# Kernel tuning notes

Measured on AMD Instinct MI355X. Metric: run time of the kernel, lower is better.

The kernel has to match this reference:

```python
import jax, jax.numpy as jnp
import numpy as np

LAMBDA_TEMP = 20.0
GAMMA = 20.0
MARGIN = 0.05
EPS = 1e-8

B, K, M, D = 128, 256, 8, 128


def _unit(x, axis=-1):
    return x / jnp.linalg.norm(x, axis=axis, keepdims=True)


def setup_inputs() -> dict:
    key = jax.random.key(0)
    k1, k2, k3 = jax.random.split(key, 3)
    v_proj = _unit(jax.random.normal(k1, (B, K, D), dtype=jnp.float32))
    prototypes = _unit(jax.random.normal(k2, (K, M, D), dtype=jnp.float32))
    concept_labels = jax.random.randint(k3, (B, K), 0, 2, dtype=jnp.int64)
    return {"v_proj": v_proj, "concept_labels": concept_labels, "prototypes": prototypes}


def reference(v_proj, concept_labels, prototypes):
    # all-pairs prototype similarities: query vector (b,k) vs prototypes of concept c
    # sims: (B, K, C, M)
    sims = jnp.einsum('bkd,cmd->bkcm', v_proj, prototypes)
    # Eq.6: soft assignment over the M prototypes of each concept
    q = jax.nn.softmax(GAMMA * sims, axis=-1)
    # Eq.7-8: weighted similarity sim_c(v)  -> (B, K, C)
    sim = jnp.sum(q * sims, axis=-1)
    # positive similarity: concept k queried against its own prototypes, plus margin
    sim_pos = jnp.einsum('bkk->bk', sim) + MARGIN  # (B, K)
    # Eq.9: -log( exp(lam*sim_pos) / (sum_c exp(lam*sim_c) + eps) )
    denom = jnp.sum(jnp.exp(LAMBDA_TEMP * sim), axis=-1) + EPS  # (B, K)
    loss_bk = jnp.log(denom) - LAMBDA_TEMP * sim_pos  # (B, K)
    mask = (concept_labels == 1).astype(loss_bk.dtype)
    num_pos = jnp.sum(mask)
    total = jnp.sum(loss_bk * mask)
    return jnp.where(num_pos > 0, total / num_pos, total)
```

## Files before the change

### kernel.cpp

```cpp
#include <hip/hip_runtime.h>

#define NROWS 32768
#define LT 20.0f
#define CHUNKS 16

typedef _Float16 half8 __attribute__((ext_vector_type(8)));
typedef float    f32x4 __attribute__((ext_vector_type(4)));

__device__ __forceinline__ float swz16(float x) {
    return __int_as_float(__builtin_amdgcn_ds_swizzle(__float_as_int(x), 0x401F));
}

#define GLD16(gp, lp) __builtin_amdgcn_global_load_lds( \
    (const __attribute__((address_space(1))) void*)(gp), \
    (__attribute__((address_space(3))) void*)(lp), 16, 0, 0)

__global__ __launch_bounds__(256)
void mpcl_prep(const float* __restrict__ P, _Float16* __restrict__ Pw)
{
    int id   = blockIdx.x * 256 + threadIdx.x;
    int gcol = id >> 4;
    int dblk = id & 15;
    int ch   = gcol >> 7;
    int col  = gcol & 127;
    int key  = (col & 3) | ((col & 8) >> 1);
    int dbs  = (dblk & 8) | ((dblk ^ key) & 7);
    const float* src = P + (size_t)gcol * 128 + dblk * 8;
    float4 a = *(const float4*)src;
    float4 b = *(const float4*)(src + 4);
    half8 hv;
    hv[0] = (_Float16)a.x; hv[1] = (_Float16)a.y;
    hv[2] = (_Float16)a.z; hv[3] = (_Float16)a.w;
    hv[4] = (_Float16)b.x; hv[5] = (_Float16)b.y;
    hv[6] = (_Float16)b.z; hv[7] = (_Float16)b.w;
    *(half8*)&Pw[((size_t)ch * 2048 + col * 16 + dbs) * 8] = hv;
}

__global__ __launch_bounds__(1024)
void mpcl_main(const float* __restrict__ V,
               const int*   __restrict__ labels,
               const _Float16* __restrict__ Pw,
               int* __restrict__ ws,
               float* __restrict__ out)
{
    __shared__ __align__(16) _Float16 Pst[2][2048 * 8];
    __shared__ float sh_denom[128];
    __shared__ float sh_simpos[128];
    __shared__ float sh_red[32];

    int*   gcnt = ws;
    float* gsum = (float*)(ws + 2);

    const int tid  = threadIdx.x;
    const int lane = tid & 63;
    const int w    = tid >> 6;
    const int rg   = w >> 2;
    const int colq = w & 3;
    const int n    = lane & 15;
    const int q    = lane >> 4;
    const int rowbase = blockIdx.x * 128;

    if (tid < 128) { sh_denom[tid] = 0.0f; sh_simpos[tid] = 0.0f; }

    half8 vh[2][4];
#pragma unroll
    for (int rf = 0; rf < 2; ++rf) {
        const float* vr = V + (size_t)(rowbase + rg * 32 + rf * 16 + n) * 128 + q * 8;
#pragma unroll
        for (int c = 0; c < 4; ++c) {
            float4 x0 = *(const float4*)(vr + c * 32);
            float4 x1 = *(const float4*)(vr + c * 32 + 4);
            vh[rf][c][0] = (_Float16)x0.x; vh[rf][c][1] = (_Float16)x0.y;
            vh[rf][c][2] = (_Float16)x0.z; vh[rf][c][3] = (_Float16)x0.w;
            vh[rf][c][4] = (_Float16)x1.x; vh[rf][c][5] = (_Float16)x1.y;
            vh[rf][c][6] = (_Float16)x1.z; vh[rf][c][7] = (_Float16)x1.w;
        }
    }

    const int col1 = colq * 32 + ((n >> 2) << 3) + (n & 3);
    int off1[4];
#pragma unroll
    for (int c = 0; c < 4; ++c) {
        int dblk = c * 4 + q;
        int dbs  = (dblk & 8) | ((dblk ^ (n & 7)) & 7);
        off1[c]  = (col1 * 16 + dbs) * 8;
    }

    const _Float16* gbase = Pw + (size_t)(w * 128 + lane) * 8;
    _Float16* l0 = &Pst[0][(w * 128) * 8];
    _Float16* l1 = &Pst[1][(w * 128) * 8];

    GLD16(gbase,       l0);
    GLD16(gbase + 512, l0 + 512);

    const int rowk0 = (rowbase + rg * 32 + n) & 255;
    const int rowk1 = (rowbase + rg * 32 + 16 + n) & 255;

    float dn[2] = {0.f, 0.f};

#pragma unroll 1
    for (int ch = 0; ch < CHUNKS; ++ch) {
        __syncthreads();

        if (ch < CHUNKS - 1) {
            const _Float16* g = gbase + (size_t)(ch + 1) * 16384;
            _Float16* lnx = (ch & 1) ? l0 : l1;
            GLD16(g,       lnx);
            GLD16(g + 512, lnx + 512);
        }

        const _Float16* base = (ch & 1) ? &Pst[1][0] : &Pst[0][0];

        f32x4 acc1[2] = {{0.f,0.f,0.f,0.f},{0.f,0.f,0.f,0.f}};
        f32x4 acc2[2] = {{0.f,0.f,0.f,0.f},{0.f,0.f,0.f,0.f}};
#pragma unroll
        for (int c = 0; c < 4; ++c) {
            half8 a1 = *(const half8*)&base[off1[c]];
            half8 a2 = *(const half8*)&base[off1[c] + 512];
            acc1[0] = __builtin_amdgcn_mfma_f32_16x16x32_f16(a1, vh[0][c], acc1[0], 0, 0, 0);
            acc1[1] = __builtin_amdgcn_mfma_f32_16x16x32_f16(a1, vh[1][c], acc1[1], 0, 0, 0);
            acc2[0] = __builtin_amdgcn_mfma_f32_16x16x32_f16(a2, vh[0][c], acc2[0], 0, 0, 0);
            acc2[1] = __builtin_amdgcn_mfma_f32_16x16x32_f16(a2, vh[1][c], acc2[1], 0, 0, 0);
        }

        const int cA = ch * 16 + colq * 4 + q;
#pragma unroll
        for (int rf = 0; rf < 2; ++rf) {
            float x0 = acc1[rf][0], x1 = acc1[rf][1], x2 = acc1[rf][2], x3 = acc1[rf][3];
            float x4 = acc2[rf][0], x5 = acc2[rf][1], x6 = acc2[rf][2], x7 = acc2[rf][3];
            float e0 = __expf(LT * x0), e1 = __expf(LT * x1);
            float e2 = __expf(LT * x2), e3 = __expf(LT * x3);
            float e4 = __expf(LT * x4), e5 = __expf(LT * x5);
            float e6 = __expf(LT * x6), e7 = __expf(LT * x7);
            float es = ((e0 + e1) + (e2 + e3)) + ((e4 + e5) + (e6 + e7));
            float ss = fmaf(e0, x0, fmaf(e1, x1, fmaf(e2, x2, e3 * x3)))
                     + fmaf(e4, x4, fmaf(e5, x5, fmaf(e6, x6, e7 * x7)));
            float simc = __fdividef(ss, es);
            dn[rf] += __expf(LT * simc);
            if (cA == (rf ? rowk1 : rowk0))
                sh_simpos[rg * 32 + rf * 16 + n] = simc;
        }
    }

#pragma unroll
    for (int rf = 0; rf < 2; ++rf) {
        float t = dn[rf];
        t += swz16(t);
        t += __shfl_xor(t, 32);
        if (lane < 16)
            atomicAdd(&sh_denom[rg * 32 + rf * 16 + n], t);
    }
    __syncthreads();

    float s = 0.f, cc = 0.f;
    if (tid < 128) {
        int row = rowbase + tid;
        float lp = logf(sh_denom[tid] + 1e-8f) - LT * (sh_simpos[tid] + 0.05f);
        float mk = (labels[row] == 1) ? 1.0f : 0.0f;
        s = lp * mk;
        cc = mk;
    }
#pragma unroll
    for (int off = 32; off >= 1; off >>= 1) {
        s  += __shfl_down(s, off);
        cc += __shfl_down(cc, off);
    }
    if (lane == 0) { sh_red[w] = s; sh_red[16 + w] = cc; }
    __syncthreads();
    if (tid == 0) {
        s = 0.f; cc = 0.f;
#pragma unroll
        for (int i = 0; i < 16; ++i) { s += sh_red[i]; cc += sh_red[16 + i]; }
        atomicAdd(&gsum[0], s);
        atomicAdd(&gsum[1], cc);
        __threadfence();
        int g = __hip_atomic_fetch_add(gcnt, 1,
                                       __ATOMIC_ACQ_REL, __HIP_MEMORY_SCOPE_AGENT);
        if (g == 255) {
            __threadfence();
            float ts = __hip_atomic_load(&gsum[0], __ATOMIC_RELAXED, __HIP_MEMORY_SCOPE_AGENT);
            float tc = __hip_atomic_load(&gsum[1], __ATOMIC_RELAXED, __HIP_MEMORY_SCOPE_AGENT);
            out[0] = (tc > 0.0f) ? (ts / tc) : ts;
        }
    }
}

extern "C" void kernel_launch(void* const* d_in, const int* in_sizes, int n_in,
                              void* d_out, int out_size, void* d_ws, size_t ws_size,
                              hipStream_t stream)
{
    const float* V      = (const float*)d_in[0];
    const int*   labels = (const int*)d_in[1];
    const float* P      = (const float*)d_in[2];
    float* out = (float*)d_out;
    int*   ws  = (int*)d_ws;
    _Float16* Pw = (_Float16*)((char*)d_ws + 512);

    hipMemsetAsync(ws, 0, 16, stream);
    mpcl_prep<<<128, 256, 0, stream>>>(P, Pw);
    mpcl_main<<<256, 1024, 0, stream>>>(V, labels, Pw, ws, out);
}
```

Baseline: 110.4 us.

## Halve block size to 512 threads and double grid to 512 blocks

Each block now handles 64 rows with 8 waves instead of 128 rows with 16 waves. Every wave issues four async global-to-LDS loads per chunk, up from two, so the prototype tile is still fully staged, and an explicit vmcnt drain is added before each barrier. The final reduction drops the shared-memory stage and has the first wave atomically add its partial sums. Similarities are also clamped to [-4,4] before the exp, a safeguard for valid unit vectors. The intent is more, smaller blocks for better occupancy and latency hiding, at the cost of twice as many per-block prototype reloads and global atomics.

```diff
diff --git a/kernel.cpp b/kernel.cpp
--- a/kernel.cpp
+++ b/kernel.cpp
@@ -1,8 +1,8 @@
 #include <hip/hip_runtime.h>
 
-#define NROWS 32768
 #define LT 20.0f
 #define CHUNKS 16
+#define NBLK 512
 
 typedef _Float16 half8 __attribute__((ext_vector_type(8)));
 typedef float    f32x4 __attribute__((ext_vector_type(4)));
@@ -14,6 +14,8 @@
 #define GLD16(gp, lp) __builtin_amdgcn_global_load_lds( \
     (const __attribute__((address_space(1))) void*)(gp), \
     (__attribute__((address_space(3))) void*)(lp), 16, 0, 0)
+
+#define VM_DRAIN() asm volatile("s_waitcnt vmcnt(0)" ::: "memory")
 
 __global__ __launch_bounds__(256)
 void mpcl_prep(const float* __restrict__ P, _Float16* __restrict__ Pw)
@@ -36,20 +38,16 @@
     *(half8*)&Pw[((size_t)ch * 2048 + col * 16 + dbs) * 8] = hv;
 }
 
-__global__ __launch_bounds__(1024)
+__global__ __launch_bounds__(512)
 void mpcl_main(const float* __restrict__ V,
                const int*   __restrict__ labels,
                const _Float16* __restrict__ Pw,
-               int* __restrict__ ws,
+               int* __restrict__ gcnt, float* __restrict__ gsum,
                float* __restrict__ out)
 {
-    __shared__ __align__(16) _Float16 Pst[2][2048 * 8];
-    __shared__ float sh_denom[128];
-    __shared__ float sh_simpos[128];
-    __shared__ float sh_red[32];
-
-    int*   gcnt = ws;
-    float* gsum = (float*)(ws + 2);
+    __shared__ __align__(16) _Float16 Pst[2][16384];
+    __shared__ float sh_denom[64];
+    __shared__ float sh_simpos[64];
 
     const int tid  = threadIdx.x;
     const int lane = tid & 63;
@@ -58,9 +56,9 @@
     const int colq = w & 3;
     const int n    = lane & 15;
     const int q    = lane >> 4;
-    const int rowbase = blockIdx.x * 128;
-
-    if (tid < 128) { sh_denom[tid] = 0.0f; sh_simpos[tid] = 0.0f; }
+    const int rowbase = blockIdx.x * 64;
+
+    if (tid < 64) { sh_denom[tid] = 0.0f; sh_simpos[tid] = 0.0f; }
 
     half8 vh[2][4];
 #pragma unroll
@@ -86,12 +84,11 @@
         off1[c]  = (col1 * 16 + dbs) * 8;
     }
 
-    const _Float16* gbase = Pw + (size_t)(w * 128 + lane) * 8;
-    _Float16* l0 = &Pst[0][(w * 128) * 8];
-    _Float16* l1 = &Pst[1][(w * 128) * 8];
-
-    GLD16(gbase,       l0);
-    GLD16(gbase + 512, l0 + 512);
+    const _Float16* gb = Pw + (size_t)w * 2048 + (size_t)lane * 8;
+    _Float16* l0 = &Pst[0][w * 2048];
+    _Float16* l1 = &Pst[1][w * 2048];
+#pragma unroll
+    for (int s = 0; s < 4; ++s) GLD16(gb + s * 512, l0 + s * 512);
 
     const int rowk0 = (rowbase + rg * 32 + n) & 255;
     const int rowk1 = (rowbase + rg * 32 + 16 + n) & 255;
@@ -100,13 +97,14 @@
 
 #pragma unroll 1
     for (int ch = 0; ch < CHUNKS; ++ch) {
+        VM_DRAIN();
         __syncthreads();
 
         if (ch < CHUNKS - 1) {
-            const _Float16* g = gbase + (size_t)(ch + 1) * 16384;
+            const _Float16* g = gb + (size_t)(ch + 1) * 16384;
             _Float16* lnx = (ch & 1) ? l0 : l1;
-            GLD16(g,       lnx);
-            GLD16(g + 512, lnx + 512);
+#pragma unroll
+            for (int s = 0; s < 4; ++s) GLD16(g + s * 512, lnx + s * 512);
         }
 
         const _Float16* base = (ch & 1) ? &Pst[1][0] : &Pst[0][0];
@@ -126,8 +124,10 @@
         const int cA = ch * 16 + colq * 4 + q;
 #pragma unroll
         for (int rf = 0; rf < 2; ++rf) {
-            float x0 = acc1[rf][0], x1 = acc1[rf][1], x2 = acc1[rf][2], x3 = acc1[rf][3];
-            float x4 = acc2[rf][0], x5 = acc2[rf][1], x6 = acc2[rf][2], x7 = acc2[rf][3];
+            float x0 = fminf(fmaxf(acc1[rf][0], -4.f), 4.f), x1 = fminf(fmaxf(acc1[rf][1], -4.f), 4.f);
+            float x2 = fminf(fmaxf(acc1[rf][2], -4.f), 4.f), x3 = fminf(fmaxf(acc1[rf][3], -4.f), 4.f);
+            float x4 = fminf(fmaxf(acc2[rf][0], -4.f), 4.f), x5 = fminf(fmaxf(acc2[rf][1], -4.f), 4.f);
+            float x6 = fminf(fmaxf(acc2[rf][2], -4.f), 4.f), x7 = fminf(fmaxf(acc2[rf][3], -4.f), 4.f);
             float e0 = __expf(LT * x0), e1 = __expf(LT * x1);
             float e2 = __expf(LT * x2), e3 = __expf(LT * x3);
             float e4 = __expf(LT * x4), e5 = __expf(LT * x5);
@@ -152,31 +152,28 @@
     }
     __syncthreads();
 
-    float s = 0.f, cc = 0.f;
-    if (tid < 128) {
+    if (tid < 64) {
         int row = rowbase + tid;
         float lp = logf(sh_denom[tid] + 1e-8f) - LT * (sh_simpos[tid] + 0.05f);
         float mk = (labels[row] == 1) ? 1.0f : 0.0f;
-        s = lp * mk;
-        cc = mk;
-    }
-#pragma unroll
-    for (int off = 32; off >= 1; off >>= 1) {
-        s  += __shfl_down(s, off);
-        cc += __shfl_down(cc, off);
-    }
-    if (lane == 0) { sh_red[w] = s; sh_red[16 + w] = cc; }
-    __syncthreads();
+        float s  = lp * mk;
+        float cc = mk;
+#pragma unroll
+        for (int off = 32; off >= 1; off >>= 1) {
+            s  += __shfl_down(s, off);
+            cc += __shfl_down(cc, off);
+        }
+        if (lane == 0) {
+            atomicAdd(&gsum[0], s);
+            atomicAdd(&gsum[1], cc);
+        }
+    }
+
     if (tid == 0) {
-        s = 0.f; cc = 0.f;
-#pragma unroll
-        for (int i = 0; i < 16; ++i) { s += sh_red[i]; cc += sh_red[16 + i]; }
-        atomicAdd(&gsum[0], s);
-        atomicAdd(&gsum[1], cc);
         __threadfence();
         int g = __hip_atomic_fetch_add(gcnt, 1,
                                        __ATOMIC_ACQ_REL, __HIP_MEMORY_SCOPE_AGENT);
-        if (g == 255) {
+        if (g == NBLK - 1) {
             __threadfence();
             float ts = __hip_atomic_load(&gsum[0], __ATOMIC_RELAXED, __HIP_MEMORY_SCOPE_AGENT);
             float tc = __hip_atomic_load(&gsum[1], __ATOMIC_RELAXED, __HIP_MEMORY_SCOPE_AGENT);
@@ -193,10 +190,13 @@
     const int*   labels = (const int*)d_in[1];
     const float* P      = (const float*)d_in[2];
     float* out = (float*)d_out;
-    int*   ws  = (int*)d_ws;
-    _Float16* Pw = (_Float16*)((char*)d_ws + 512);
-
-    hipMemsetAsync(ws, 0, 16, stream);
+
+    int*   wsi  = (int*)d_ws;
+    int*   gcnt = wsi;
+    float* gsum = (float*)(wsi + 2);
+    _Float16* Pw = (_Float16*)((char*)d_ws + 64);
+
+    hipMemsetAsync(d_ws, 0, 64, stream);
     mpcl_prep<<<128, 256, 0, stream>>>(P, Pw);
-    mpcl_main<<<256, 1024, 0, stream>>>(V, labels, Pw, ws, out);
-}
+    mpcl_main<<<NBLK, 512, 0, stream>>>(V, labels, Pw, gcnt, gsum, out);
+}
```

Measured after the change: 119.8 us. +8.5%, slower.
